# Kernel tuning notes

Hardware: AMD Instinct MI355X
Metric: run time of the kernel (lower is better)

## Reference

```python
import jax, jax.numpy as jnp
import numpy as np

N_NODES = 100000
N_EDGES = 800000
EPS = 1e-5


def _mean_agg(h, src, dst):
    # DGL SAGEConv 'mean': average of in-neighbor features per dst node.
    msg = jnp.take(h, src, axis=0)                      # [E, D] gather
    summed = jax.ops.segment_sum(msg, dst, num_segments=N_NODES)
    deg = jax.ops.segment_sum(jnp.ones((src.shape[0],), h.dtype), dst,
                              num_segments=N_NODES)
    return summed / jnp.maximum(deg, 1.0)[:, None]


def _sage(h, src, dst, ws, wn, b):
    # rst = fc_self(h) + fc_neigh(mean_neigh) + bias
    return h @ ws + _mean_agg(h, src, dst) @ wn + b


def _bn(x, g, b, m, v):
    return (x - m) * (g / jnp.sqrt(v + EPS)) + b


def setup_inputs() -> dict:
    key = jax.random.key(0)
    ks = jax.random.split(key, 16)
    s = 0.02
    inp = {
        "structural_features": jax.random.normal(ks[0], (N_NODES, 128), jnp.float32),
        "multimodal_features": jax.random.normal(ks[1], (N_NODES, 384), jnp.float32),
        "src": jax.random.randint(ks[2], (N_EDGES,), 0, N_NODES),
        "dst": jax.random.randint(ks[3], (N_EDGES,), 0, N_NODES),
        "enc_w": jax.random.normal(ks[4], (512, 128), jnp.float32) * s,
        "enc_b": jnp.zeros((128,), jnp.float32),
        "sage0_ws": jax.random.normal(ks[5], (128, 256), jnp.float32) * s,
        "sage0_wn": jax.random.normal(ks[6], (128, 256), jnp.float32) * s,
        "sage0_b": jnp.zeros((256,), jnp.float32),
        "bn0_g": jnp.ones((256,), jnp.float32),
        "bn0_b": jnp.zeros((256,), jnp.float32),
        "bn0_m": jnp.zeros((256,), jnp.float32),
        "bn0_v": jnp.ones((256,), jnp.float32),
        "sage1_ws": jax.random.normal(ks[7], (256, 128), jnp.float32) * s,
        "sage1_wn": jax.random.normal(ks[8], (256, 128), jnp.float32) * s,
        "sage1_b": jnp.zeros((128,), jnp.float32),
        "bn1_g": jnp.ones((128,), jnp.float32),
        "bn1_b": jnp.zeros((128,), jnp.float32),
        "bn1_m": jnp.zeros((128,), jnp.float32),
        "bn1_v": jnp.ones((128,), jnp.float32),
        "rel_w": jax.random.normal(ks[9], (256, 128), jnp.float32) * s,
        "rel_b": jnp.zeros((128,), jnp.float32),
        "cls_w1": jax.random.normal(ks[10], (128, 64), jnp.float32) * s,
        "cls_b1": jnp.zeros((64,), jnp.float32),
        "cls_w2": jax.random.normal(ks[11], (64, 32), jnp.float32) * s,
        "cls_b2": jnp.zeros((32,), jnp.float32),
    }
    return inp


def reference(structural_features, multimodal_features, src, dst,
              enc_w, enc_b,
              sage0_ws, sage0_wn, sage0_b, bn0_g, bn0_b, bn0_m, bn0_v,
              sage1_ws, sage1_wn, sage1_b, bn1_g, bn1_b, bn1_m, bn1_v,
              rel_w, rel_b, cls_w1, cls_b1, cls_w2, cls_b2):
    x = jnp.concatenate([structural_features, multimodal_features], axis=-1)
    h0 = jax.nn.relu(x @ enc_w + enc_b)                     # input_encoder (dropout=eval)
    h = jax.nn.relu(_bn(_sage(h0, src, dst, sage0_ws, sage0_wn, sage0_b),
                        bn0_g, bn0_b, bn0_m, bn0_v))
    h = jax.nn.relu(_bn(_sage(h, src, dst, sage1_ws, sage1_wn, sage1_b),
                        bn1_g, bn1_b, bn1_m, bn1_v))
    h_final = jnp.concatenate([h0, h], axis=1)              # [N, 256]
    h_final = jax.nn.relu(h_final @ rel_w + rel_b)          # relation_encoder
    out = jax.nn.relu(h_final @ cls_w1 + cls_b1) @ cls_w2 + cls_b2
    return out
```

## Files before the change

### kernel.cpp

```cpp
#include <hip/hip_runtime.h>
#include <math.h>


#define EPS 1e-5f

typedef __attribute__((ext_vector_type(8))) short bf16x8;
typedef __attribute__((ext_vector_type(4))) float f32x4;

__device__ inline unsigned short f2bf(float x) {
    unsigned u = __float_as_uint(x);
    u += 0x7fff + ((u >> 16) & 1);
    return (unsigned short)(u >> 16);
}
__device__ inline float bf2f(unsigned short h) {
    return __uint_as_float(((unsigned)h) << 16);
}
__device__ inline unsigned packbf(float x, float y) {
    return (unsigned)f2bf(x) | ((unsigned)f2bf(y) << 16);
}

__device__ inline void gload_lds16(const void* g, void* l) {
    __builtin_amdgcn_global_load_lds(
        (__attribute__((address_space(1))) void*)g,
        (__attribute__((address_space(3))) void*)l, 16, 0, 0);
}


__global__ void count_deg(const int* __restrict__ dst, int* __restrict__ deg, int e) {
    int i = blockIdx.x * 256 + threadIdx.x;
    if (i < e) atomicAdd(&deg[dst[i]], 1);
}

__global__ __launch_bounds__(1024)
void scan_block(const int* __restrict__ deg, int* __restrict__ rowptr,
                int* __restrict__ part, int n) {
    __shared__ int buf[1024];
    const int tid = threadIdx.x;
    const int i = blockIdx.x * 1024 + tid;
    const int v = (i < n) ? deg[i] : 0;
    buf[tid] = v;
    __syncthreads();
    #pragma unroll 1
    for (int off = 1; off < 1024; off <<= 1) {
        int t = (tid >= off) ? buf[tid - off] : 0;
        __syncthreads();
        buf[tid] += t;
        __syncthreads();
    }
    if (i < n) rowptr[i] = buf[tid] - v;
    if (tid == 1023) part[blockIdx.x] = buf[1023];
}

__global__ __launch_bounds__(1024)
void scan_part(int* __restrict__ part, int nb) {
    __shared__ int buf[1024];
    const int tid = threadIdx.x;
    const int v = (tid < nb) ? part[tid] : 0;
    buf[tid] = v;
    __syncthreads();
    #pragma unroll 1
    for (int off = 1; off < 1024; off <<= 1) {
        int t = (tid >= off) ? buf[tid - off] : 0;
        __syncthreads();
        buf[tid] += t;
        __syncthreads();
    }
    if (tid < nb) part[tid] = buf[tid] - v;
    if (tid == 1023) part[nb] = buf[1023];
}

__global__ void scan_add(const int* __restrict__ part, int* __restrict__ rowptr,
                         int* __restrict__ cursor, int n, int nb) {
    int i = blockIdx.x * 256 + threadIdx.x;
    if (i < n) {
        int v = rowptr[i] + part[i >> 10];
        rowptr[i] = v;
        cursor[i] = v;
    }
    if (i == 0) rowptr[n] = part[nb];
}

__global__ void fill_edges(const int* __restrict__ src, const int* __restrict__ dst,
                           int* __restrict__ cursor, int* __restrict__ eidx, int e) {
    int i = blockIdx.x * 256 + threadIdx.x;
    if (i < e) {
        int pos = atomicAdd(&cursor[dst[i]], 1);
        eidx[pos] = src[i];
    }
}


__global__ __launch_bounds__(256)
void prep_all(const float* __restrict__ enc_w, const float* __restrict__ s0_ws,
              const float* __restrict__ s0_wn, const float* __restrict__ s1_ws,
              const float* __restrict__ s1_wn, const float* __restrict__ rel_w,
              const float* __restrict__ cw1, const float* __restrict__ cw2,
              short* wt_enc_h, short* wt_enc_l, short* wt_s0_h, short* wt_s0_l,
              short* wt_st_h, short* wt_st_l, short* wt_rel_h, short* wt_rel_l,
              short* wt_c1_h, short* wt_c1_l, short* wt_c2_h, short* wt_c2_l) {
    int e = blockIdx.x * 256 + threadIdx.x;
    const float* W; short* hi; short* lo; int Nd, ldt, koff;
    if (e < 65536)       { W = enc_w; hi = wt_enc_h; lo = wt_enc_l; Nd = 128; ldt = 512; koff = 0; }
    else if (e < 98304)  { e -= 65536;  W = s0_ws; hi = wt_s0_h; lo = wt_s0_l; Nd = 256; ldt = 256; koff = 0; }
    else if (e < 131072) { e -= 98304;  W = s0_wn; hi = wt_s0_h; lo = wt_s0_l; Nd = 256; ldt = 256; koff = 128; }
    else if (e < 163840) { e -= 131072; W = s1_ws; hi = wt_st_h; lo = wt_st_l; Nd = 128; ldt = 256; koff = 0; }
    else if (e < 196608) { e -= 163840; W = s1_wn; hi = wt_st_h + 32768; lo = wt_st_l + 32768; Nd = 128; ldt = 256; koff = 0; }
    else if (e < 229376) { e -= 196608; W = rel_w; hi = wt_rel_h; lo = wt_rel_l; Nd = 128; ldt = 256; koff = 0; }
    else if (e < 237568) { e -= 229376; W = cw1; hi = wt_c1_h; lo = wt_c1_l; Nd = 64; ldt = 128; koff = 0; }
    else if (e < 239616) { e -= 237568; W = cw2; hi = wt_c2_h; lo = wt_c2_l; Nd = 32; ldt = 64; koff = 0; }
    else return;
    const int k = e / Nd, n = e - k * Nd;
    const float x = W[e];
    const unsigned short h = f2bf(x);
    const unsigned short l = f2bf(x - bf2f(h));
    const size_t o = (size_t)n * ldt + koff + k;
    hi[o] = (short)h;
    lo[o] = (short)l;
}


__global__ __launch_bounds__(256)
void agg_mean_bb(const short* __restrict__ featb,
                 const int* __restrict__ rowptr, const int* __restrict__ eidx,
                 short* __restrict__ outb, int n) {
    const int node = blockIdx.x * 4 + (threadIdx.x >> 6);
    if (node >= n) return;
    const int lane = threadIdx.x & 63;
    const int g = lane >> 4, j = lane & 15;
    const int beg = rowptr[node], end = rowptr[node + 1];
    float s[8];
    #pragma unroll
    for (int i = 0; i < 8; ++i) s[i] = 0.f;
    for (int e = beg + g; e < end; e += 8) {
        const int e1 = e + 4;
        const bool has2 = e1 < end;
        const int i0 = eidx[e];
        const int i1 = has2 ? eidx[e1] : i0;
        const uint4 v0 = *(const uint4*)(featb + (size_t)i0 * 128 + j * 8);
        const uint4 v1 = *(const uint4*)(featb + (size_t)i1 * 128 + j * 8);
        __builtin_amdgcn_sched_barrier(0);
        s[0] += __uint_as_float(v0.x << 16); s[1] += __uint_as_float(v0.x & 0xffff0000u);
        s[2] += __uint_as_float(v0.y << 16); s[3] += __uint_as_float(v0.y & 0xffff0000u);
        s[4] += __uint_as_float(v0.z << 16); s[5] += __uint_as_float(v0.z & 0xffff0000u);
        s[6] += __uint_as_float(v0.w << 16); s[7] += __uint_as_float(v0.w & 0xffff0000u);
        if (has2) {
            s[0] += __uint_as_float(v1.x << 16); s[1] += __uint_as_float(v1.x & 0xffff0000u);
            s[2] += __uint_as_float(v1.y << 16); s[3] += __uint_as_float(v1.y & 0xffff0000u);
            s[4] += __uint_as_float(v1.z << 16); s[5] += __uint_as_float(v1.z & 0xffff0000u);
            s[6] += __uint_as_float(v1.w << 16); s[7] += __uint_as_float(v1.w & 0xffff0000u);
        }
    }
    #pragma unroll
    for (int i = 0; i < 8; ++i) {
        s[i] += __shfl_xor(s[i], 32);
        s[i] += __shfl_xor(s[i], 16);
    }
    if (g == 0) {
        const float inv = 1.0f / fmaxf((float)(end - beg), 1.0f);
        uint4 o;
        o.x = packbf(s[0] * inv, s[1] * inv);
        o.y = packbf(s[2] * inv, s[3] * inv);
        o.z = packbf(s[4] * inv, s[5] * inv);
        o.w = packbf(s[6] * inv, s[7] * inv);
        *(uint4*)(outb + (size_t)node * 128 + j * 8) = o;
    }
}

__global__ __launch_bounds__(256)
void agg_combine_bb(const short* __restrict__ featb,
                    const int* __restrict__ rowptr, const int* __restrict__ eidx,
                    const float* __restrict__ s1,
                    const float* __restrict__ bias,
                    const float* __restrict__ bng, const float* __restrict__ bnb,
                    const float* __restrict__ bnm, const float* __restrict__ bnv,
                    short* __restrict__ outb, int n) {
    const int node = blockIdx.x * 4 + (threadIdx.x >> 6);
    if (node >= n) return;
    const int lane = threadIdx.x & 63;
    const int g = lane >> 4, j = lane & 15;
    const int beg = rowptr[node], end = rowptr[node + 1];
    float s[8];
    #pragma unroll
    for (int i = 0; i < 8; ++i) s[i] = 0.f;
    for (int e = beg + g; e < end; e += 8) {
        const int e1 = e + 4;
        const bool has2 = e1 < end;
        const int i0 = eidx[e];
        const int i1 = has2 ? eidx[e1] : i0;
        const uint4 v0 = *(const uint4*)(featb + (size_t)i0 * 128 + j * 8);
        const uint4 v1 = *(const uint4*)(featb + (size_t)i1 * 128 + j * 8);
        __builtin_amdgcn_sched_barrier(0);
        s[0] += __uint_as_float(v0.x << 16); s[1] += __uint_as_float(v0.x & 0xffff0000u);
        s[2] += __uint_as_float(v0.y << 16); s[3] += __uint_as_float(v0.y & 0xffff0000u);
        s[4] += __uint_as_float(v0.z << 16); s[5] += __uint_as_float(v0.z & 0xffff0000u);
        s[6] += __uint_as_float(v0.w << 16); s[7] += __uint_as_float(v0.w & 0xffff0000u);
        if (has2) {
            s[0] += __uint_as_float(v1.x << 16); s[1] += __uint_as_float(v1.x & 0xffff0000u);
            s[2] += __uint_as_float(v1.y << 16); s[3] += __uint_as_float(v1.y & 0xffff0000u);
            s[4] += __uint_as_float(v1.z << 16); s[5] += __uint_as_float(v1.z & 0xffff0000u);
            s[6] += __uint_as_float(v1.w << 16); s[7] += __uint_as_float(v1.w & 0xffff0000u);
        }
    }
    #pragma unroll
    for (int i = 0; i < 8; ++i) {
        s[i] += __shfl_xor(s[i], 32);
        s[i] += __shfl_xor(s[i], 16);
    }
    if (g == 0) {
        const float inv = 1.0f / fmaxf((float)(end - beg), 1.0f);
        const int c0 = j * 8;
        const float4 a0 = *(const float4*)(s1 + (size_t)node * 128 + c0);
        const float4 a1 = *(const float4*)(s1 + (size_t)node * 128 + c0 + 4);
        const float sf[8] = {a0.x, a0.y, a0.z, a0.w, a1.x, a1.y, a1.z, a1.w};
        float r[8];
        #pragma unroll
        for (int i = 0; i < 8; ++i) {
            const int c = c0 + i;
            float v = sf[i] + s[i] * inv + bias[c];
            v = (v - bnm[c]) * (bng[c] / sqrtf(bnv[c] + EPS)) + bnb[c];
            r[i] = fmaxf(v, 0.f);
        }
        uint4 o;
        o.x = packbf(r[0], r[1]); o.y = packbf(r[2], r[3]);
        o.z = packbf(r[4], r[5]); o.w = packbf(r[6], r[7]);
        *(uint4*)(outb + (size_t)node * 128 + j * 8) = o;
    }
}

template<int NT, int K1, int K2>
__global__ __launch_bounds__(256)
void gemm_dp(const short* __restrict__ A1, int lda1,
             const short* __restrict__ A2, int lda2,
             const short* __restrict__ Wt_hi, const short* __restrict__ Wt_lo,
             const float* __restrict__ bias,
             const float* __restrict__ bng, const float* __restrict__ bnb,
             const float* __restrict__ bnm, const float* __restrict__ bnv,
             int relu,
             float* __restrict__ Cf, int fpN, int ldc,
             short* __restrict__ Cb, int bfcol0, int ldcb,
             int M) {
    constexpr int K   = K1 + K2;
    constexpr int NBK = K / 64;
    constexpr int NTW = NT / 2;
    static_assert(K % 64 == 0, "K multiple of 64");
    static_assert(NT % 2 == 0, "NT even");
    static_assert(K2 == 0 || K1 % 64 == 0, "concat boundary on BK");
    constexpr int ASZ = 128 * 64;
    constexpr int BSZ = 2 * NT * 16 * 64;
    constexpr int BUF = ASZ + BSZ;
    __shared__ short lds[2 * BUF];

    const int tid  = threadIdx.x;
    const int lane = tid & 63;
    const int wv   = tid >> 6;
    const int wm   = wv >> 1;
    const int wn   = wv & 1;
    const int bm   = blockIdx.y * 128;
    const int col0 = blockIdx.x * (NT * 16);
    const int lrow = lane & 15;
    const int quad = lane >> 4;

    const int su = (tid & 7) ^ ((tid >> 3) & 7);
    const short* gsA1[4];
    const short* gsA2[4];
    #pragma unroll
    for (int jj = 0; jj < 4; ++jj) {
        const int rg = min(bm + jj * 32 + (tid >> 3), M - 1);
        gsA1[jj] = A1 + (size_t)rg * lda1 + su * 8;
        if constexpr (K2 > 0) gsA2[jj] = A2 + (size_t)rg * lda2 + su * 8;
        else gsA2[jj] = nullptr;
    }
    const short* gsB[NT];
    #pragma unroll
    for (int jj = 0; jj < NT; ++jj) {
        const int colIdx = jj * 32 + (tid >> 3);
        const bool ishi = colIdx < NT * 16;
        const int cp = ishi ? colIdx : colIdx - NT * 16;
        gsB[jj] = (ishi ? Wt_hi : Wt_lo) + (size_t)(col0 + cp) * K + su * 8;
    }

    auto stage = [&](int b, int c) {
        const int k = c * 64;
        #pragma unroll
        for (int jj = 0; jj < 4; ++jj) {
            const short* p;
            if constexpr (K2 > 0)
                p = (k < K1) ? (gsA1[jj] + k) : (gsA2[jj] + (k - K1));
            else
                p = gsA1[jj] + k;
            gload_lds16(p, &lds[b * BUF + (jj * 256 + tid) * 8]);
        }
        #pragma unroll
        for (int jj = 0; jj < NT; ++jj)
            gload_lds16(gsB[jj] + k, &lds[b * BUF + ASZ + (jj * 256 + tid) * 8]);
    };

    int aoff[4][2];
    #pragma unroll
    for (int m = 0; m < 4; ++m)
        #pragma unroll
        for (int kk = 0; kk < 2; ++kk)
            aoff[m][kk] = (wm * 64 + m * 16 + lrow) * 64 +
                          (((kk * 4 + quad) ^ (lrow & 7)) * 8);
    int boff[NTW][2];
    #pragma unroll
    for (int nt = 0; nt < NTW; ++nt)
        #pragma unroll
        for (int kk = 0; kk < 2; ++kk)
            boff[nt][kk] = (wn * NTW * 16 + nt * 16 + lrow) * 64 +
                           (((kk * 4 + quad) ^ (lrow & 7)) * 8);

    f32x4 acc[4][NTW];
    #pragma unroll
    for (int m = 0; m < 4; ++m)
        #pragma unroll
        for (int nt = 0; nt < NTW; ++nt)
            acc[m][nt] = (f32x4){0.f, 0.f, 0.f, 0.f};

    stage(0, 0);

    for (int c = 0; c < NBK; ++c) {
        const int b = c & 1;
        if (c + 1 < NBK) {
            stage(b ^ 1, c + 1);
            if constexpr (NT == 4) asm volatile("s_waitcnt vmcnt(8)" ::: "memory");
            else                   asm volatile("s_waitcnt vmcnt(6)" ::: "memory");
        } else {
            asm volatile("s_waitcnt vmcnt(0)" ::: "memory");
        }
        __builtin_amdgcn_s_barrier();

        const short* La = &lds[b * BUF];
        const short* Lb = &lds[b * BUF + ASZ];
        #pragma unroll
        for (int kk = 0; kk < 2; ++kk) {
            bf16x8 a[4];
            #pragma unroll
            for (int m = 0; m < 4; ++m)
                a[m] = *(const bf16x8*)(La + aoff[m][kk]);
            #pragma unroll
            for (int nt = 0; nt < NTW; ++nt) {
                const bf16x8 vbh = *(const bf16x8*)(Lb + boff[nt][kk]);
                const bf16x8 vbl = *(const bf16x8*)(Lb + boff[nt][kk] + NT * 16 * 64);
                #pragma unroll
                for (int m = 0; m < 4; ++m) {
                    acc[m][nt] = __builtin_amdgcn_mfma_f32_16x16x32_bf16(a[m], vbh, acc[m][nt], 0, 0, 0);
                    acc[m][nt] = __builtin_amdgcn_mfma_f32_16x16x32_bf16(a[m], vbl, acc[m][nt], 0, 0, 0);
                }
            }
        }
        asm volatile("" ::: "memory");
        __builtin_amdgcn_s_barrier();
    }

    constexpr int EW = NT * 16 + 4;
    float* ep = (float*)lds;

    #pragma unroll
    for (int nt = 0; nt < NTW; ++nt) {
        const int lcol = wn * NTW * 16 + nt * 16 + lrow;
        const int gcol = col0 + lcol;
        const float bsc = bias ? bias[gcol] : 0.f;
        float gg = 1.f, bb = 0.f, mm = 0.f;
        if (bng) { gg = bng[gcol] / sqrtf(bnv[gcol] + EPS); bb = bnb[gcol]; mm = bnm[gcol]; }
        #pragma unroll
        for (int m = 0; m < 4; ++m) {
            #pragma unroll
            for (int r = 0; r < 4; ++r) {
                float x = acc[m][nt][r] + bsc;
                if (bng) x = (x - mm) * gg + bb;
                if (relu) x = fmaxf(x, 0.f);
                ep[(wm * 64 + m * 16 + quad * 4 + r) * EW + lcol] = x;
            }
        }
    }
    __syncthreads();

    if (col0 < fpN) {
        for (int g = tid; g < 128 * NT * 4; g += 256) {
            const int row = g / (NT * 4), u = g - row * (NT * 4);
            const int grow = bm + row;
            if (grow < M)
                *(float4*)(Cf + (size_t)grow * ldc + col0 + u * 4) =
                    *(const float4*)(ep + row * EW + u * 4);
        }
    } else {
        for (int g = tid; g < 128 * NT * 2; g += 256) {
            const int row = g / (NT * 2), u = g - row * (NT * 2);
            const int grow = bm + row;
            const float4 f0 = *(const float4*)(ep + row * EW + u * 8);
            const float4 f1 = *(const float4*)(ep + row * EW + u * 8 + 4);
            uint4 o;
            o.x = packbf(f0.x, f0.y); o.y = packbf(f0.z, f0.w);
            o.z = packbf(f1.x, f1.y); o.w = packbf(f1.z, f1.w);
            if (grow < M)
                *(uint4*)(Cb + (size_t)grow * ldcb + (col0 - bfcol0) + u * 8) = o;
        }
    }
}

__global__ __launch_bounds__(256)
void gemm_enc(const float* __restrict__ A1f,
              const float* __restrict__ A2f,
              const short* __restrict__ Wt_hi, const short* __restrict__ Wt_lo,
              const float* __restrict__ bias,
              short* __restrict__ Cb, int ldcb, int M) {
    constexpr int NT = 4, NTW = 2, K = 512, NBK = 8;
    constexpr int ASZ = 128 * 64;
    constexpr int BSZ = 2 * NT * 16 * 64;
    constexpr int BUF = ASZ + BSZ;
    __shared__ short lds[2 * BUF];

    const int tid  = threadIdx.x;
    const int lane = tid & 63;
    const int wv   = tid >> 6;
    const int wm   = wv >> 1;
    const int wn   = wv & 1;
    const int bm   = blockIdx.y * 128;
    const int col0 = blockIdx.x * (NT * 16);
    const int lrow = lane & 15;
    const int quad = lane >> 4;

    const int su = (tid & 7) ^ ((tid >> 3) & 7);
    const float* gsA1[4];
    const float* gsA2[4];
    #pragma unroll
    for (int jj = 0; jj < 4; ++jj) {
        const int rg = min(bm + jj * 32 + (tid >> 3), M - 1);
        gsA1[jj] = A1f + (size_t)rg * 128 + su * 8;
        gsA2[jj] = A2f + (size_t)rg * 384 + su * 8;
    }
    const short* gsB[NT];
    #pragma unroll
    for (int jj = 0; jj < NT; ++jj) {
        const int colIdx = jj * 32 + (tid >> 3);
        const bool ishi = colIdx < NT * 16;
        const int cp = ishi ? colIdx : colIdx - NT * 16;
        gsB[jj] = (ishi ? Wt_hi : Wt_lo) + (size_t)(col0 + cp) * K + su * 8;
    }
    auto stageB = [&](int b, int c) {
        const int k = c * 64;
        #pragma unroll
        for (int jj = 0; jj < NT; ++jj)
            gload_lds16(gsB[jj] + k, &lds[b * BUF + ASZ + (jj * 256 + tid) * 8]);
    };

    int aoff[4][2], boff[NTW][2];
    #pragma unroll
    for (int m = 0; m < 4; ++m)
        #pragma unroll
        for (int kk = 0; kk < 2; ++kk)
            aoff[m][kk] = (wm * 64 + m * 16 + lrow) * 64 +
                          (((kk * 4 + quad) ^ (lrow & 7)) * 8);
    #pragma unroll
    for (int nt = 0; nt < NTW; ++nt)
        #pragma unroll
        for (int kk = 0; kk < 2; ++kk)
            boff[nt][kk] = (wn * NTW * 16 + nt * 16 + lrow) * 64 +
                           (((kk * 4 + quad) ^ (lrow & 7)) * 8);

    f32x4 acc[4][NTW];
    #pragma unroll
    for (int m = 0; m < 4; ++m)
        #pragma unroll
        for (int nt = 0; nt < NTW; ++nt)
            acc[m][nt] = (f32x4){0.f, 0.f, 0.f, 0.f};

    float4 awin[8];

    #pragma unroll
    for (int jj = 0; jj < 4; ++jj) {
        awin[jj * 2 + 0] = *(const float4*)(gsA1[jj]);
        awin[jj * 2 + 1] = *(const float4*)(gsA1[jj] + 4);
    }
    stageB(0, 0);
    #pragma unroll
    for (int jj = 0; jj < 4; ++jj) {
        const float4 w0 = awin[jj * 2 + 0], w1 = awin[jj * 2 + 1];
        uint4 o;
        o.x = packbf(w0.x, w0.y); o.y = packbf(w0.z, w0.w);
        o.z = packbf(w1.x, w1.y); o.w = packbf(w1.z, w1.w);
        *((uint4*)&lds[(jj * 256 + tid) * 8]) = o;
    }
    asm volatile("s_waitcnt vmcnt(0)" ::: "memory");
    __builtin_amdgcn_s_barrier();

    #pragma unroll
    for (int c = 0; c < NBK; ++c) {
        const int cur = c & 1, nxt = cur ^ 1;
        if (c + 1 < NBK) {
            const int k1 = (c + 1) * 64;
            #pragma unroll
            for (int jj = 0; jj < 4; ++jj) {
                const float* p = (k1 < 128) ? (gsA1[jj] + k1)
                                            : (gsA2[jj] + (k1 - 128));
                awin[jj * 2 + 0] = *(const float4*)p;
                awin[jj * 2 + 1] = *(const float4*)(p + 4);
            }
            stageB(nxt, c + 1);
            __builtin_amdgcn_sched_barrier(0);
        }

        const short* La = &lds[cur * BUF];
        const short* Lb = &lds[cur * BUF + ASZ];
        #pragma unroll
        for (int kk = 0; kk < 2; ++kk) {
            bf16x8 a[4];
            #pragma unroll
            for (int m = 0; m < 4; ++m)
                a[m] = *(const bf16x8*)(La + aoff[m][kk]);
            #pragma unroll
            for (int nt = 0; nt < NTW; ++nt) {
                const bf16x8 vbh = *(const bf16x8*)(Lb + boff[nt][kk]);
                const bf16x8 vbl = *(const bf16x8*)(Lb + boff[nt][kk] + NT * 16 * 64);
                #pragma unroll
                for (int m = 0; m < 4; ++m) {
                    acc[m][nt] = __builtin_amdgcn_mfma_f32_16x16x32_bf16(a[m], vbh, acc[m][nt], 0, 0, 0);
                    acc[m][nt] = __builtin_amdgcn_mfma_f32_16x16x32_bf16(a[m], vbl, acc[m][nt], 0, 0, 0);
                }
            }
        }

        if (c + 1 < NBK) {
            #pragma unroll
            for (int jj = 0; jj < 4; ++jj) {
                const float4 w0 = awin[jj * 2 + 0], w1 = awin[jj * 2 + 1];
                uint4 o;
                o.x = packbf(w0.x, w0.y); o.y = packbf(w0.z, w0.w);
                o.z = packbf(w1.x, w1.y); o.w = packbf(w1.z, w1.w);
                *((uint4*)&lds[nxt * BUF + (jj * 256 + tid) * 8]) = o;
            }
            asm volatile("s_waitcnt vmcnt(0)" ::: "memory");
            __builtin_amdgcn_s_barrier();
        }
    }
    __builtin_amdgcn_s_barrier();

    constexpr int EW = NT * 16 + 4;
    float* ep = (float*)lds;
    #pragma unroll
    for (int nt = 0; nt < NTW; ++nt) {
        const int lcol = wn * NTW * 16 + nt * 16 + lrow;
        const float bsc = bias[col0 + lcol];
        #pragma unroll
        for (int m = 0; m < 4; ++m)
            #pragma unroll
            for (int r = 0; r < 4; ++r)
                ep[(wm * 64 + m * 16 + quad * 4 + r) * EW + lcol] =
                    fmaxf(acc[m][nt][r] + bsc, 0.f);
    }
    __syncthreads();
    for (int g = tid; g < 128 * NT * 2; g += 256) {
        const int row = g / (NT * 2), u = g - row * (NT * 2);
        const int grow = bm + row;
        const float4 f0 = *(const float4*)(ep + row * EW + u * 8);
        const float4 f1 = *(const float4*)(ep + row * EW + u * 8 + 4);
        uint4 o;
        o.x = packbf(f0.x, f0.y); o.y = packbf(f0.z, f0.w);
        o.z = packbf(f1.x, f1.y); o.w = packbf(f1.z, f1.w);
        if (grow < M)
            *(uint4*)(Cb + (size_t)grow * ldcb + col0 + u * 8) = o;
    }
}

__global__ __launch_bounds__(256)
void gemm_relcls(const short* __restrict__ A1,
                 const short* __restrict__ A2,
                 const short* __restrict__ Wh, const short* __restrict__ Wl,
                 const float* __restrict__ rel_b,
                 const short* __restrict__ W1h, const short* __restrict__ W1l,
                 const float* __restrict__ cb1,
                 const short* __restrict__ W2h, const short* __restrict__ W2l,
                 const float* __restrict__ cb2,
                 float* __restrict__ out, int M) {
    constexpr int NT = 8, NTW = 4, NBK = 4, K = 256;
    constexpr int ASZ = 128 * 64;
    constexpr int BSZ = 2 * NT * 16 * 64;
    constexpr int BUF = ASZ + BSZ;
    __shared__ short lds[2 * BUF];

    const int tid  = threadIdx.x;
    const int lane = tid & 63;
    const int wv   = tid >> 6;
    const int wm   = wv >> 1;
    const int wn   = wv & 1;
    const int bm   = blockIdx.x * 128;
    const int lrow = lane & 15;
    const int quad = lane >> 4;

    const int su = (tid & 7) ^ ((tid >> 3) & 7);
    const short* gsA1[4];
    const short* gsA2[4];
    #pragma unroll
    for (int jj = 0; jj < 4; ++jj) {
        const int rg = min(bm + jj * 32 + (tid >> 3), M - 1);
        gsA1[jj] = A1 + (size_t)rg * 128 + su * 8;
        gsA2[jj] = A2 + (size_t)rg * 128 + su * 8;
    }
    const short* gsB[NT];
    #pragma unroll
    for (int jj = 0; jj < NT; ++jj) {
        const int colIdx = jj * 32 + (tid >> 3);
        const bool ishi = colIdx < 128;
        const int cp = ishi ? colIdx : colIdx - 128;
        gsB[jj] = (ishi ? Wh : Wl) + (size_t)cp * K + su * 8;
    }
    auto stage = [&](int b, int c) {
        const int k = c * 64;
        #pragma unroll
        for (int jj = 0; jj < 4; ++jj) {
            const short* p = (k < 128) ? (gsA1[jj] + k) : (gsA2[jj] + (k - 128));
            gload_lds16(p, &lds[b * BUF + (jj * 256 + tid) * 8]);
        }
        #pragma unroll
        for (int jj = 0; jj < NT; ++jj)
            gload_lds16(gsB[jj] + k, &lds[b * BUF + ASZ + (jj * 256 + tid) * 8]);
    };

    int aoff[4][2], boff[NTW][2];
    #pragma unroll
    for (int m = 0; m < 4; ++m)
        #pragma unroll
        for (int kk = 0; kk < 2; ++kk)
            aoff[m][kk] = (wm * 64 + m * 16 + lrow) * 64 +
                          (((kk * 4 + quad) ^ (lrow & 7)) * 8);
    #pragma unroll
    for (int nt = 0; nt < NTW; ++nt)
        #pragma unroll
        for (int kk = 0; kk < 2; ++kk)
            boff[nt][kk] = (wn * 64 + nt * 16 + lrow) * 64 +
                           (((kk * 4 + quad) ^ (lrow & 7)) * 8);

    f32x4 acc[4][NTW];
    #pragma unroll
    for (int m = 0; m < 4; ++m)
        #pragma unroll
        for (int nt = 0; nt < NTW; ++nt)
            acc[m][nt] = (f32x4){0.f, 0.f, 0.f, 0.f};

    stage(0, 0);
    for (int c = 0; c < NBK; ++c) {
        const int b = c & 1;
        if (c + 1 < NBK) {
            stage(b ^ 1, c + 1);
            asm volatile("s_waitcnt vmcnt(12)" ::: "memory");
        } else {
            asm volatile("s_waitcnt vmcnt(0)" ::: "memory");
        }
        __builtin_amdgcn_s_barrier();

        const short* La = &lds[b * BUF];
        const short* Lb = &lds[b * BUF + ASZ];
        #pragma unroll
        for (int kk = 0; kk < 2; ++kk) {
            bf16x8 a[4];
            #pragma unroll
            for (int m = 0; m < 4; ++m)
                a[m] = *(const bf16x8*)(La + aoff[m][kk]);
            #pragma unroll
            for (int nt = 0; nt < NTW; ++nt) {
                const bf16x8 vbh = *(const bf16x8*)(Lb + boff[nt][kk]);
                const bf16x8 vbl = *(const bf16x8*)(Lb + boff[nt][kk] + 128 * 64);
                #pragma unroll
                for (int m = 0; m < 4; ++m) {
                    acc[m][nt] = __builtin_amdgcn_mfma_f32_16x16x32_bf16(a[m], vbh, acc[m][nt], 0, 0, 0);
                    acc[m][nt] = __builtin_amdgcn_mfma_f32_16x16x32_bf16(a[m], vbl, acc[m][nt], 0, 0, 0);
                }
            }
        }
        asm volatile("" ::: "memory");
        __builtin_amdgcn_s_barrier();
    }

    constexpr int EW1 = 132;
    float* rt = (float*)lds;
    #pragma unroll
    for (int nt = 0; nt < NTW; ++nt) {
        const int lcol = wn * 64 + nt * 16 + lrow;
        const float bsc = rel_b[lcol];
        #pragma unroll
        for (int m = 0; m < 4; ++m)
            #pragma unroll
            for (int r = 0; r < 4; ++r)
                rt[(wm * 64 + m * 16 + quad * 4 + r) * EW1 + lcol] =
                    fmaxf(acc[m][nt][r] + bsc, 0.f);
    }
    __syncthreads();

    f32x4 acc2[4][2];
    #pragma unroll
    for (int m = 0; m < 4; ++m)
        #pragma unroll
        for (int nt = 0; nt < 2; ++nt)
            acc2[m][nt] = (f32x4){0.f, 0.f, 0.f, 0.f};
    #pragma unroll
    for (int kk = 0; kk < 4; ++kk) {
        bf16x8 b2h[2], b2l[2];
        #pragma unroll
        for (int nt = 0; nt < 2; ++nt) {
            const size_t cw = (size_t)(wn * 32 + nt * 16 + lrow) * 128 + kk * 32 + quad * 8;
            b2h[nt] = *(const bf16x8*)(W1h + cw);
            b2l[nt] = *(const bf16x8*)(W1l + cw);
        }
        #pragma unroll
        for (int m = 0; m < 4; ++m) {
            const float* pe = rt + (wm * 64 + m * 16 + lrow) * EW1 + kk * 32 + quad * 8;
            const float4 e0 = *(const float4*)pe;
            const float4 e1 = *(const float4*)(pe + 4);
            bf16x8 a;
            a[0] = (short)f2bf(e0.x); a[1] = (short)f2bf(e0.y);
            a[2] = (short)f2bf(e0.z); a[3] = (short)f2bf(e0.w);
            a[4] = (short)f2bf(e1.x); a[5] = (short)f2bf(e1.y);
            a[6] = (short)f2bf(e1.z); a[7] = (short)f2bf(e1.w);
            #pragma unroll
            for (int nt = 0; nt < 2; ++nt) {
                acc2[m][nt] = __builtin_amdgcn_mfma_f32_16x16x32_bf16(a, b2h[nt], acc2[m][nt], 0, 0, 0);
                acc2[m][nt] = __builtin_amdgcn_mfma_f32_16x16x32_bf16(a, b2l[nt], acc2[m][nt], 0, 0, 0);
            }
        }
    }
    __syncthreads();

    constexpr int EW2 = 68;
    float* ep2 = (float*)lds;
    #pragma unroll
    for (int nt = 0; nt < 2; ++nt) {
        const int lcol = wn * 32 + nt * 16 + lrow;
        const float bsc = cb1[lcol];
        #pragma unroll
        for (int m = 0; m < 4; ++m)
            #pragma unroll
            for (int r = 0; r < 4; ++r)
                ep2[(wm * 64 + m * 16 + quad * 4 + r) * EW2 + lcol] =
                    fmaxf(acc2[m][nt][r] + bsc, 0.f);
    }
    __syncthreads();

    const short* pB3h = W2h + (size_t)(wn * 16 + lrow) * 64 + quad * 8;
    const short* pB3l = W2l + (size_t)(wn * 16 + lrow) * 64 + quad * 8;
    f32x4 acc3[4];
    #pragma unroll
    for (int m = 0; m < 4; ++m) acc3[m] = (f32x4){0.f, 0.f, 0.f, 0.f};
    #pragma unroll
    for (int kk = 0; kk < 2; ++kk) {
        const bf16x8 bh = *(const bf16x8*)(pB3h + kk * 32);
        const bf16x8 bl = *(const bf16x8*)(pB3l + kk * 32);
        #pragma unroll
        for (int m = 0; m < 4; ++m) {
            const float* pe = ep2 + (wm * 64 + m * 16 + lrow) * EW2 + kk * 32 + quad * 8;
            const float4 e0 = *(const float4*)pe;
            const float4 e1 = *(const float4*)(pe + 4);
            bf16x8 a;
            a[0] = (short)f2bf(e0.x); a[1] = (short)f2bf(e0.y);
            a[2] = (short)f2bf(e0.z); a[3] = (short)f2bf(e0.w);
            a[4] = (short)f2bf(e1.x); a[5] = (short)f2bf(e1.y);
            a[6] = (short)f2bf(e1.z); a[7] = (short)f2bf(e1.w);
            acc3[m] = __builtin_amdgcn_mfma_f32_16x16x32_bf16(a, bh, acc3[m], 0, 0, 0);
            acc3[m] = __builtin_amdgcn_mfma_f32_16x16x32_bf16(a, bl, acc3[m], 0, 0, 0);
        }
    }

    constexpr int EW3 = 36;
    float* ep3 = (float*)lds + 128 * EW2;
    {
        const int lcol = wn * 16 + lrow;
        const float bsc = cb2[lcol];
        #pragma unroll
        for (int m = 0; m < 4; ++m)
            #pragma unroll
            for (int r = 0; r < 4; ++r)
                ep3[(wm * 64 + m * 16 + quad * 4 + r) * EW3 + lcol] =
                    acc3[m][r] + bsc;
    }
    __syncthreads();
    #pragma unroll
    for (int j = 0; j < 4; ++j) {
        const int g = tid + j * 256;
        const int row = g >> 3, u = g & 7;
        const int grow = bm + row;
        if (grow < M)
            *(float4*)(out + (size_t)grow * 32 + u * 4) =
                *(const float4*)(ep3 + row * EW3 + u * 4);
    }
}


extern "C" void kernel_launch(void* const* d_in, const int* in_sizes, int n_in,
                              void* d_out, int out_size, void* d_ws, size_t ws_size,
                              hipStream_t stream) {
    const float* sf    = (const float*)d_in[0];
    const float* mf    = (const float*)d_in[1];
    const int*   src   = (const int*)d_in[2];
    const int*   dst   = (const int*)d_in[3];
    const float* enc_w = (const float*)d_in[4];
    const float* enc_b = (const float*)d_in[5];
    const float* s0_ws = (const float*)d_in[6];
    const float* s0_wn = (const float*)d_in[7];
    const float* s0_b  = (const float*)d_in[8];
    const float* bn0_g = (const float*)d_in[9];
    const float* bn0_b = (const float*)d_in[10];
    const float* bn0_m = (const float*)d_in[11];
    const float* bn0_v = (const float*)d_in[12];
    const float* s1_ws = (const float*)d_in[13];
    const float* s1_wn = (const float*)d_in[14];
    const float* s1_b  = (const float*)d_in[15];
    const float* bn1_g = (const float*)d_in[16];
    const float* bn1_b = (const float*)d_in[17];
    const float* bn1_m = (const float*)d_in[18];
    const float* bn1_v = (const float*)d_in[19];
    const float* rel_w = (const float*)d_in[20];
    const float* rel_b = (const float*)d_in[21];
    const float* cw1   = (const float*)d_in[22];
    const float* cb1   = (const float*)d_in[23];
    const float* cw2   = (const float*)d_in[24];
    const float* cb2   = (const float*)d_in[25];
    float* out = (float*)d_out;

    const int nn = in_sizes[0] / 128;
    const int ne = in_sizes[2];
    const int nb = (nn + 1023) / 1024;

    short* h0b   = (short*)d_ws;
    short* xb    = h0b + (size_t)nn * 128;
    float* st    = (float*)xb;
    short* h1b   = (short*)(st + (size_t)nn * 128);
    short* agg0b = xb + (size_t)nn * 512;
    short* t1b   = agg0b + (size_t)nn * 128;
    short* h2b   = t1b + (size_t)nn * 128;
    int* deg    = (int*)(h2b + (size_t)nn * 128);
    int* rowptr = deg + nn;
    int* cursor = rowptr + nn + 1;
    int* part   = cursor + nn;
    int* eidx   = part + nb + 1;
    short* wts = (short*)(eidx + ne);
    short* wt_enc_h = wts;                 short* wt_enc_l = wt_enc_h + 65536;
    short* wt_s0_h  = wt_enc_l + 65536;    short* wt_s0_l  = wt_s0_h  + 65536;
    short* wt_st_h  = wt_s0_l  + 65536;    short* wt_st_l  = wt_st_h  + 65536;
    short* wt_rel_h = wt_st_l  + 65536;    short* wt_rel_l = wt_rel_h + 32768;
    short* wt_c1_h  = wt_rel_l + 32768;    short* wt_c1_l  = wt_c1_h  + 8192;
    short* wt_c2_h  = wt_c1_l  + 8192;     short* wt_c2_l  = wt_c2_h  + 2048;

    const dim3 blk(256);
    const int gM = (nn + 127) / 128;

    hipMemsetAsync(deg, 0, (size_t)nn * 4, stream);
    count_deg <<<dim3((ne + 255) / 256), blk, 0, stream>>>(dst, deg, ne);
    scan_block<<<dim3(nb), dim3(1024), 0, stream>>>(deg, rowptr, part, nn);
    scan_part <<<dim3(1),  dim3(1024), 0, stream>>>(part, nb);
    scan_add  <<<dim3((nn + 255) / 256), blk, 0, stream>>>(part, rowptr, cursor, nn, nb);
    fill_edges<<<dim3((ne + 255) / 256), blk, 0, stream>>>(src, dst, cursor, eidx, ne);

    prep_all<<<dim3(936), blk, 0, stream>>>(
        enc_w, s0_ws, s0_wn, s1_ws, s1_wn, rel_w, cw1, cw2,
        wt_enc_h, wt_enc_l, wt_s0_h, wt_s0_l, wt_st_h, wt_st_l,
        wt_rel_h, wt_rel_l, wt_c1_h, wt_c1_l, wt_c2_h, wt_c2_l);

    gemm_enc<<<dim3(2, gM), blk, 0, stream>>>(
        sf, mf, wt_enc_h, wt_enc_l, enc_b, h0b, 128, nn);

    agg_mean_bb<<<dim3((nn + 3) / 4), blk, 0, stream>>>(
        h0b, rowptr, eidx, agg0b, nn);

    gemm_dp<4, 128, 128><<<dim3(4, gM), blk, 0, stream>>>(
        h0b, 128, agg0b, 128, wt_s0_h, wt_s0_l, s0_b,
        bn0_g, bn0_b, bn0_m, bn0_v, 1,
        nullptr, 0, 0, h1b, 0, 256, nn);

    gemm_dp<4, 256, 0><<<dim3(4, gM), blk, 0, stream>>>(
        h1b, 256, nullptr, 0, wt_st_h, wt_st_l, nullptr,
        nullptr, nullptr, nullptr, nullptr, 0,
        st, 128, 128, t1b, 128, 128, nn);

    agg_combine_bb<<<dim3((nn + 3) / 4), blk, 0, stream>>>(
        t1b, rowptr, eidx, st, s1_b,
        bn1_g, bn1_b, bn1_m, bn1_v, h2b, nn);

    gemm_relcls<<<dim3(gM), blk, 0, stream>>>(
        h0b, h2b, wt_rel_h, wt_rel_l, rel_b,
        wt_c1_h, wt_c1_l, cb1, wt_c2_h, wt_c2_l, cb2, out, nn);
}
```

Baseline: 659.4 us.

## Widen GEMM tiles to 128 columns with 512-thread blocks

Replaces the 256-thread, 64-column GEMM kernel with a 512-thread variant that computes 128x128 output tiles using 8 waves in a 2x4 layout. Each block now loads its A rows once for twice as many output columns, which halves A-tile reloads across column blocks and the grid size. In exchange the kernel uses more LDS per block (the B buffers double) and more threads per block, which may lower occupancy.

```diff
diff --git a/kernel.cpp b/kernel.cpp
--- a/kernel.cpp
+++ b/kernel.cpp
@@ -227,23 +227,22 @@
     }
 }
 
-template<int NT, int K1, int K2>
-__global__ __launch_bounds__(256)
-void gemm_dp(const short* __restrict__ A1, int lda1,
-             const short* __restrict__ A2, int lda2,
-             const short* __restrict__ Wt_hi, const short* __restrict__ Wt_lo,
-             const float* __restrict__ bias,
-             const float* __restrict__ bng, const float* __restrict__ bnb,
-             const float* __restrict__ bnm, const float* __restrict__ bnv,
-             int relu,
-             float* __restrict__ Cf, int fpN, int ldc,
-             short* __restrict__ Cb, int bfcol0, int ldcb,
-             int M) {
+template<int K1, int K2>
+__global__ __launch_bounds__(512)
+void gemm_w(const short* __restrict__ A1, int lda1,
+            const short* __restrict__ A2, int lda2,
+            const short* __restrict__ Wt_hi, const short* __restrict__ Wt_lo,
+            const float* __restrict__ bias,
+            const float* __restrict__ bng, const float* __restrict__ bnb,
+            const float* __restrict__ bnm, const float* __restrict__ bnv,
+            int relu,
+            float* __restrict__ Cf, int fpN, int ldc,
+            short* __restrict__ Cb, int bfcol0, int ldcb,
+            int M) {
     constexpr int K   = K1 + K2;
     constexpr int NBK = K / 64;
-    constexpr int NTW = NT / 2;
+    constexpr int NT  = 8, NTW = 2;
     static_assert(K % 64 == 0, "K multiple of 64");
-    static_assert(NT % 2 == 0, "NT even");
     static_assert(K2 == 0 || K1 % 64 == 0, "concat boundary on BK");
     constexpr int ASZ = 128 * 64;
     constexpr int BSZ = 2 * NT * 16 * 64;
@@ -253,46 +252,46 @@
     const int tid  = threadIdx.x;
     const int lane = tid & 63;
     const int wv   = tid >> 6;
-    const int wm   = wv >> 1;
-    const int wn   = wv & 1;
+    const int wm   = wv >> 2;
+    const int wn   = wv & 3;
     const int bm   = blockIdx.y * 128;
-    const int col0 = blockIdx.x * (NT * 16);
+    const int col0 = blockIdx.x * 128;
     const int lrow = lane & 15;
     const int quad = lane >> 4;
 
     const int su = (tid & 7) ^ ((tid >> 3) & 7);
-    const short* gsA1[4];
-    const short* gsA2[4];
-    #pragma unroll
-    for (int jj = 0; jj < 4; ++jj) {
-        const int rg = min(bm + jj * 32 + (tid >> 3), M - 1);
+    const short* gsA1[2];
+    const short* gsA2[2];
+    #pragma unroll
+    for (int jj = 0; jj < 2; ++jj) {
+        const int rg = min(bm + jj * 64 + (tid >> 3), M - 1);
         gsA1[jj] = A1 + (size_t)rg * lda1 + su * 8;
         if constexpr (K2 > 0) gsA2[jj] = A2 + (size_t)rg * lda2 + su * 8;
         else gsA2[jj] = nullptr;
     }
-    const short* gsB[NT];
-    #pragma unroll
-    for (int jj = 0; jj < NT; ++jj) {
-        const int colIdx = jj * 32 + (tid >> 3);
-        const bool ishi = colIdx < NT * 16;
-        const int cp = ishi ? colIdx : colIdx - NT * 16;
+    const short* gsB[4];
+    #pragma unroll
+    for (int jj = 0; jj < 4; ++jj) {
+        const int colIdx = jj * 64 + (tid >> 3);
+        const bool ishi = colIdx < 128;
+        const int cp = ishi ? colIdx : colIdx - 128;
         gsB[jj] = (ishi ? Wt_hi : Wt_lo) + (size_t)(col0 + cp) * K + su * 8;
     }
 
     auto stage = [&](int b, int c) {
         const int k = c * 64;
         #pragma unroll
-        for (int jj = 0; jj < 4; ++jj) {
+        for (int jj = 0; jj < 2; ++jj) {
             const short* p;
             if constexpr (K2 > 0)
                 p = (k < K1) ? (gsA1[jj] + k) : (gsA2[jj] + (k - K1));
             else
                 p = gsA1[jj] + k;
-            gload_lds16(p, &lds[b * BUF + (jj * 256 + tid) * 8]);
-        }
-        #pragma unroll
-        for (int jj = 0; jj < NT; ++jj)
-            gload_lds16(gsB[jj] + k, &lds[b * BUF + ASZ + (jj * 256 + tid) * 8]);
+            gload_lds16(p, &lds[b * BUF + (jj * 512 + tid) * 8]);
+        }
+        #pragma unroll
+        for (int jj = 0; jj < 4; ++jj)
+            gload_lds16(gsB[jj] + k, &lds[b * BUF + ASZ + (jj * 512 + tid) * 8]);
     };
 
     int aoff[4][2];
@@ -307,7 +306,7 @@
     for (int nt = 0; nt < NTW; ++nt)
         #pragma unroll
         for (int kk = 0; kk < 2; ++kk)
-            boff[nt][kk] = (wn * NTW * 16 + nt * 16 + lrow) * 64 +
+            boff[nt][kk] = (wn * 32 + nt * 16 + lrow) * 64 +
                            (((kk * 4 + quad) ^ (lrow & 7)) * 8);
 
     f32x4 acc[4][NTW];
@@ -323,8 +322,7 @@
         const int b = c & 1;
         if (c + 1 < NBK) {
             stage(b ^ 1, c + 1);
-            if constexpr (NT == 4) asm volatile("s_waitcnt vmcnt(8)" ::: "memory");
-            else                   asm volatile("s_waitcnt vmcnt(6)" ::: "memory");
+            asm volatile("s_waitcnt vmcnt(6)" ::: "memory");
         } else {
             asm volatile("s_waitcnt vmcnt(0)" ::: "memory");
         }
@@ -353,12 +351,12 @@
         __builtin_amdgcn_s_barrier();
     }
 
-    constexpr int EW = NT * 16 + 4;
+    constexpr int EW = 132;
     float* ep = (float*)lds;
 
     #pragma unroll
     for (int nt = 0; nt < NTW; ++nt) {
-        const int lcol = wn * NTW * 16 + nt * 16 + lrow;
+        const int lcol = wn * 32 + nt * 16 + lrow;
         const int gcol = col0 + lcol;
         const float bsc = bias ? bias[gcol] : 0.f;
         float gg = 1.f, bb = 0.f, mm = 0.f;
@@ -377,16 +375,16 @@
     __syncthreads();
 
     if (col0 < fpN) {
-        for (int g = tid; g < 128 * NT * 4; g += 256) {
-            const int row = g / (NT * 4), u = g - row * (NT * 4);
+        for (int g = tid; g < 128 * 32; g += 512) {
+            const int row = g >> 5, u = g & 31;
             const int grow = bm + row;
             if (grow < M)
                 *(float4*)(Cf + (size_t)grow * ldc + col0 + u * 4) =
                     *(const float4*)(ep + row * EW + u * 4);
         }
     } else {
-        for (int g = tid; g < 128 * NT * 2; g += 256) {
-            const int row = g / (NT * 2), u = g - row * (NT * 2);
+        for (int g = tid; g < 128 * 16; g += 512) {
+            const int row = g >> 4, u = g & 15;
             const int grow = bm + row;
             const float4 f0 = *(const float4*)(ep + row * EW + u * 8);
             const float4 f1 = *(const float4*)(ep + row * EW + u * 8 + 4);
@@ -841,6 +839,7 @@
     short* wt_c2_h  = wt_c1_l  + 8192;     short* wt_c2_l  = wt_c2_h  + 2048;
 
     const dim3 blk(256);
+    const dim3 blk512(512);
     const int gM = (nn + 127) / 128;
 
     hipMemsetAsync(deg, 0, (size_t)nn * 4, stream);
@@ -861,12 +860,12 @@
     agg_mean_bb<<<dim3((nn + 3) / 4), blk, 0, stream>>>(
         h0b, rowptr, eidx, agg0b, nn);
 
-    gemm_dp<4, 128, 128><<<dim3(4, gM), blk, 0, stream>>>(
+    gemm_w<128, 128><<<dim3(2, gM), blk512, 0, stream>>>(
         h0b, 128, agg0b, 128, wt_s0_h, wt_s0_l, s0_b,
         bn0_g, bn0_b, bn0_m, bn0_v, 1,
         nullptr, 0, 0, h1b, 0, 256, nn);
 
-    gemm_dp<4, 256, 0><<<dim3(4, gM), blk, 0, stream>>>(
+    gemm_w<256, 0><<<dim3(2, gM), blk512, 0, stream>>>(
         h1b, 256, nullptr, 0, wt_st_h, wt_st_l, nullptr,
         nullptr, nullptr, nullptr, nullptr, 0,
         st, 128, 128, t1b, 128, 128, nn);
```

After: 669.5 us. No clear change (+1.5%).
